# Kernel optimization log

Hardware: AMD Instinct MI355X
Metric: run time of the kernel (lower is better)

Reference implementation:

```python
import jax, jax.numpy as jnp
import numpy as np

N_USERS = 100000
N_ITEMS = 50000
N_NODES = N_USERS + N_ITEMS
EMB_DIM = 64
N_EDGES = 4000000
N_LAYERS = 3
BATCH = 4096


def setup_inputs() -> dict:
    key = jax.random.key(0)
    k = jax.random.split(key, 7)
    return {
        "user_emb": jax.random.normal(k[0], (N_USERS, EMB_DIM), dtype=jnp.float32) * 0.1,
        "item_emb": jax.random.normal(k[1], (N_ITEMS, EMB_DIM), dtype=jnp.float32) * 0.1,
        "vals": jax.random.uniform(k[2], (N_EDGES,), dtype=jnp.float32),
        "src": jax.random.randint(k[3], (N_EDGES,), 0, N_NODES, dtype=jnp.int32),
        "dst": jax.random.randint(k[4], (N_EDGES,), 0, N_NODES, dtype=jnp.int32),
        "users": jax.random.randint(k[5], (BATCH,), 0, N_USERS, dtype=jnp.int32),
        "items": jax.random.randint(k[6], (BATCH,), 0, N_ITEMS, dtype=jnp.int32),
    }


def _propagate(user_emb, item_emb, vals, src, dst):
    # all_emb: [N, D]; sparse adjacency A given as COO (src -> dst, weight vals)
    all_emb = jnp.concatenate([user_emb, item_emb], axis=0)
    acc = all_emb  # running sum over layers (layer 0 included)
    emb = all_emb
    for _ in range(N_LAYERS):
        # SpMM: out[d] = sum_{e: dst[e]==d} vals[e] * emb[src[e]]
        msgs = vals[:, None] * emb[src]               # [E, D]
        emb = jax.ops.segment_sum(msgs, dst, num_segments=N_NODES)
        acc = acc + emb
    light_out = acc / jnp.float32(N_LAYERS + 1)       # mean over stacked layers
    return light_out[:N_USERS], light_out[N_USERS:]


def reference(user_emb, item_emb, vals, src, dst, users, items):
    all_users, all_items = _propagate(user_emb, item_emb, vals, src, dst)
    u = all_users[users]                              # [B, D]
    i = all_items[items]                              # [B, D]
    gamma = jnp.sum(u * i, axis=1)                    # [B]
    return gamma
```

## Files before the change

kernel.cpp:

```cpp
#include <hip/hip_runtime.h>
#include <hip/hip_bf16.h>

#define N_USERS 100000
#define N_ITEMS 50000
#define N_NODES 150000
#define DIM 64
#define N_EDGES 4000000
#define BATCH 4096

#define NBKT 512
#define BW 294
#define STRIDE 9216
#define PA_EDGES 4096
#define PA_ITER 16
#define PA_BLOCKS ((N_EDGES + PA_EDGES - 1) / PA_EDGES)
#define CVT_BLOCKS (N_NODES * DIM / 4 / 256)

__device__ __forceinline__ float blo(unsigned int u) { return __uint_as_float(u << 16); }
__device__ __forceinline__ float bhi(unsigned int u) { return __uint_as_float(u & 0xffff0000u); }
__device__ __forceinline__ unsigned int f2b(float f) {
    unsigned int x = __float_as_uint(f);
    return (x + 0x7fffu + ((x >> 16) & 1u)) >> 16;
}
__device__ __forceinline__ unsigned int pack2(float a, float b) {
    return f2b(a) | (f2b(b) << 16);
}

typedef float v2f __attribute__((ext_vector_type(2)));

__global__ void __launch_bounds__(256, 4) k_cvtpart(
        const float* __restrict__ uemb, const float* __restrict__ iemb,
        ushort* __restrict__ ebf0,
        const int* __restrict__ src, const int* __restrict__ dst,
        const float* __restrict__ vals,
        int* __restrict__ gcur, int2* __restrict__ tmp) {
    __shared__ int cnt[NBKT];
    __shared__ int base_s[NBKT];
    __shared__ int off_s[NBKT];
    __shared__ int2 rec_s[PA_EDGES];
    __shared__ ushort bin_s[PA_EDGES];
    int t = threadIdx.x;
    if (blockIdx.x >= PA_BLOCKS) {
        int tid = (blockIdx.x - PA_BLOCKS) * 256 + t;
        int i = tid * 4;
        if (i >= N_NODES * DIM) return;
        const float* srcp = (i < N_USERS * DIM) ? (uemb + i) : (iemb + (i - N_USERS * DIM));
        float4 v;
        v.x = __builtin_nontemporal_load(srcp + 0);
        v.y = __builtin_nontemporal_load(srcp + 1);
        v.z = __builtin_nontemporal_load(srcp + 2);
        v.w = __builtin_nontemporal_load(srcp + 3);
        *(uint2*)(ebf0 + i) = make_uint2(pack2(v.x, v.y), pack2(v.z, v.w));
        return;
    }
    for (int i = t; i < NBKT; i += 256) cnt[i] = 0;
    __syncthreads();
    size_t base = (size_t)blockIdx.x * PA_EDGES;
    int myb[PA_ITER];
    int mykey[PA_ITER];
    int myval[PA_ITER];
#pragma unroll
    for (int it = 0; it < PA_ITER; it++) {
        size_t i = base + (size_t)it * 256 + t;
        myb[it] = -1;
        if (i < N_EDGES) {
            int d = __builtin_nontemporal_load(dst + i);
            int s = __builtin_nontemporal_load(src + i);
            float v = __builtin_nontemporal_load(vals + i);
            int b = d / BW;
            int local = d - b * BW;
            myb[it] = b;
            mykey[it] = (s << 9) | local;
            myval[it] = __float_as_int(v);
            atomicAdd(&cnt[b], 1);
        }
    }
    __syncthreads();
    for (int i = t; i < NBKT; i += 256) {
        int c = cnt[i];
        base_s[i] = (c > 0) ? atomicAdd(&gcur[i], c) : 0;
    }
    if (t < 64) {
        int lane = t;
        int carry = 0;
        for (int c = 0; c < NBKT / 64; c++) {
            int i = c * 64 + lane;
            int x = cnt[i];
            int incl = x;
            for (int o = 1; o < 64; o <<= 1) {
                int y = __shfl_up(incl, o);
                if (lane >= o) incl += y;
            }
            off_s[i] = carry + incl - x;
            carry += __shfl(incl, 63);
        }
    }
    __syncthreads();
    for (int i = t; i < NBKT; i += 256) cnt[i] = 0;
    __syncthreads();
#pragma unroll
    for (int it = 0; it < PA_ITER; it++) {
        int b = myb[it];
        if (b >= 0) {
            int pos = off_s[b] + atomicAdd(&cnt[b], 1);
            rec_s[pos] = make_int2(mykey[it], myval[it]);
            bin_s[pos] = (ushort)b;
        }
    }
    __syncthreads();
    int nrec = off_s[NBKT - 1] + cnt[NBKT - 1];
    for (int i = t; i < nrec; i += 256) {
        int2 r = rec_s[i];
        int b = bin_s[i];
        tmp[(size_t)b * STRIDE + base_s[b] + (i - off_s[b])] = r;
    }
}

__global__ void k_bsort(const int2* __restrict__ tmp, const int* __restrict__ gcur,
                        int* __restrict__ row_ptr, int2* __restrict__ fin) {
    __shared__ int cnt[BW + 64];
    __shared__ int off[BW + 64];
    __shared__ int gbase_s;
    int b = blockIdx.x, t = threadIdx.x;
    int node0 = b * BW;
    int nodes = min(BW, N_NODES - node0);
    int count = gcur[b];
    const int2* tb = tmp + (size_t)b * STRIDE;
    if (t < 64) {
        int ssum = 0;
#pragma unroll
        for (int j = 0; j < 8; j++) {
            int idx = t * 8 + j;
            if (idx < b) ssum += gcur[idx];
        }
        for (int o = 32; o; o >>= 1) ssum += __shfl_xor(ssum, o);
        if (t == 0) gbase_s = ssum;
    }
    for (int i = t; i < BW + 64; i += 512) cnt[i] = 0;
    __syncthreads();
    int gbase = gbase_s;
    for (int e = t; e < count; e += 512) atomicAdd(&cnt[tb[e].x & 511], 1);
    __syncthreads();
    if (t < 64) {
        int lane = t;
        int carry = 0;
        for (int c = 0; c < 5; c++) {
            int i = c * 64 + lane;
            int x = (i < nodes) ? cnt[i] : 0;
            int incl = x;
            for (int o = 1; o < 64; o <<= 1) {
                int y = __shfl_up(incl, o);
                if (lane >= o) incl += y;
            }
            if (i <= nodes) off[i] = carry + incl - x;
            carry += __shfl(incl, 63);
        }
    }
    __syncthreads();
    for (int i = t; i <= nodes; i += 512)
        if (node0 + i <= N_NODES) row_ptr[node0 + i] = gbase + off[i];
    __syncthreads();
    for (int e = t; e < count; e += 512) {
        int2 r = tb[e];
        int local = r.x & 511;
        int pos = gbase + atomicAdd(&off[local], 1);
        fin[pos] = make_int2(r.x >> 9, r.y);
    }
}


#define EDGE_FMA(r, u, A0, A1, A2, A3)                                        \
    {                                                                         \
        float vf = __int_as_float((r).y);                                     \
        v2f vv = {vf, vf};                                                    \
        v2f f0 = {blo((u).x), bhi((u).x)};                                    \
        v2f f1 = {blo((u).y), bhi((u).y)};                                    \
        v2f f2 = {blo((u).z), bhi((u).z)};                                    \
        v2f f3 = {blo((u).w), bhi((u).w)};                                    \
        A0 = __builtin_elementwise_fma(vv, f0, A0);                           \
        A1 = __builtin_elementwise_fma(vv, f1, A1);                           \
        A2 = __builtin_elementwise_fma(vv, f2, A2);                           \
        A3 = __builtin_elementwise_fma(vv, f3, A3);                           \
    }

#define GATHER16(basec, r) (*(const uint4*)((basec) + ((((unsigned int)(r).x) << 7) | qoff)))
#define REC8(basec, i) (*(const int2*)((basec) + (((unsigned int)(i)) << 3)))

__global__ void __launch_bounds__(256) k_spmm16(
        const ushort* __restrict__ ein, ushort* __restrict__ eout,
        const int* __restrict__ row_ptr, const int2* __restrict__ fin) {
    int wave = (blockIdx.x * blockDim.x + threadIdx.x) >> 6;
    if (wave >= N_NODES / 2) return;
    int lane = threadIdx.x & 63;
    int g = lane >> 3;
    int q = lane & 7;
    unsigned int qoff = (unsigned int)q << 4;
    const char* einc = (const char*)ein;
    const char* finc = (const char*)fin;
    int n0 = wave * 2;
    int s0 = row_ptr[n0];
    int m0 = row_ptr[n0 + 1];
    int m1 = row_ptr[n0 + 2];
    int last0 = max(s0, m0 - 1);
    int last1 = max(m0, m1 - 1);
    v2f A0 = {0.f, 0.f}, A1 = {0.f, 0.f}, A2 = {0.f, 0.f}, A3 = {0.f, 0.f};
    v2f B0 = {0.f, 0.f}, B1 = {0.f, 0.f}, B2 = {0.f, 0.f}, B3 = {0.f, 0.f};
    int ea = s0 + g, eb = m0 + g;
    while (ea < m0 || eb < m1) {
        int2 ra0 = REC8(finc, min(ea, last0));
        int2 ra1 = REC8(finc, min(ea + 8, last0));
        int2 ra2 = REC8(finc, min(ea + 16, last0));
        int2 ra3 = REC8(finc, min(ea + 24, last0));
        int2 rb0 = REC8(finc, min(eb, last1));
        int2 rb1 = REC8(finc, min(eb + 8, last1));
        int2 rb2 = REC8(finc, min(eb + 16, last1));
        int2 rb3 = REC8(finc, min(eb + 24, last1));
        ra0.y = (ea < m0) ? ra0.y : 0;
        ra1.y = (ea + 8 < m0) ? ra1.y : 0;
        ra2.y = (ea + 16 < m0) ? ra2.y : 0;
        ra3.y = (ea + 24 < m0) ? ra3.y : 0;
        rb0.y = (eb < m1) ? rb0.y : 0;
        rb1.y = (eb + 8 < m1) ? rb1.y : 0;
        rb2.y = (eb + 16 < m1) ? rb2.y : 0;
        rb3.y = (eb + 24 < m1) ? rb3.y : 0;
        uint4 ua0 = GATHER16(einc, ra0);
        uint4 ua1 = GATHER16(einc, ra1);
        uint4 ua2 = GATHER16(einc, ra2);
        uint4 ua3 = GATHER16(einc, ra3);
        uint4 ub0 = GATHER16(einc, rb0);
        uint4 ub1 = GATHER16(einc, rb1);
        uint4 ub2 = GATHER16(einc, rb2);
        uint4 ub3 = GATHER16(einc, rb3);
        EDGE_FMA(ra0, ua0, A0, A1, A2, A3);
        EDGE_FMA(ra1, ua1, A0, A1, A2, A3);
        EDGE_FMA(ra2, ua2, A0, A1, A2, A3);
        EDGE_FMA(ra3, ua3, A0, A1, A2, A3);
        EDGE_FMA(rb0, ub0, B0, B1, B2, B3);
        EDGE_FMA(rb1, ub1, B0, B1, B2, B3);
        EDGE_FMA(rb2, ub2, B0, B1, B2, B3);
        EDGE_FMA(rb3, ub3, B0, B1, B2, B3);
        ea += 32;
        eb += 32;
    }
#pragma unroll
    for (int off = 8; off < 64; off <<= 1) {
        A0.x += __shfl_xor(A0.x, off);
        A0.y += __shfl_xor(A0.y, off);
        A1.x += __shfl_xor(A1.x, off);
        A1.y += __shfl_xor(A1.y, off);
        A2.x += __shfl_xor(A2.x, off);
        A2.y += __shfl_xor(A2.y, off);
        A3.x += __shfl_xor(A3.x, off);
        A3.y += __shfl_xor(A3.y, off);
        B0.x += __shfl_xor(B0.x, off);
        B0.y += __shfl_xor(B0.y, off);
        B1.x += __shfl_xor(B1.x, off);
        B1.y += __shfl_xor(B1.y, off);
        B2.x += __shfl_xor(B2.x, off);
        B2.y += __shfl_xor(B2.y, off);
        B3.x += __shfl_xor(B3.x, off);
        B3.y += __shfl_xor(B3.y, off);
    }
    if (lane < 16) {
        bool r0 = lane < 8;
        uint4 p;
        p.x = r0 ? pack2(A0.x, A0.y) : pack2(B0.x, B0.y);
        p.y = r0 ? pack2(A1.x, A1.y) : pack2(B1.x, B1.y);
        p.z = r0 ? pack2(A2.x, A2.y) : pack2(B2.x, B2.y);
        p.w = r0 ? pack2(A3.x, A3.y) : pack2(B3.x, B3.y);
        *(uint4*)(eout + (size_t)n0 * DIM + (size_t)(lane & 15) * 8) = p;
    }
}

__global__ void k_samp(const ushort* __restrict__ ein, const int* __restrict__ row_ptr,
                       const int2* __restrict__ fin, const int* __restrict__ users,
                       const int* __restrict__ items, float* __restrict__ l3) {
    int slot = (blockIdx.x * blockDim.x + threadIdx.x) >> 6;
    if (slot >= 2 * BATCH) return;
    int lane = threadIdx.x & 63;
    int g = lane >> 3;
    int q = lane & 7;
    unsigned int qoff = (unsigned int)q << 4;
    const char* einc = (const char*)ein;
    const char* finc = (const char*)fin;
    int node = (slot < BATCH) ? users[slot] : (items[slot - BATCH] + N_USERS);
    int start = row_ptr[node], end = row_ptr[node + 1];
    int last = max(start, end - 1);
    v2f A0 = {0.f, 0.f}, A1 = {0.f, 0.f}, A2 = {0.f, 0.f}, A3 = {0.f, 0.f};
    int e = start + g;
    while (e < end) {
        int e1 = e + 8, e2 = e + 16, e3 = e + 24;
        int2 ra = REC8(finc, e);
        int2 rb = REC8(finc, min(e1, last));
        int2 rc = REC8(finc, min(e2, last));
        int2 rd = REC8(finc, min(e3, last));
        rb.y = (e1 < end) ? rb.y : 0;
        rc.y = (e2 < end) ? rc.y : 0;
        rd.y = (e3 < end) ? rd.y : 0;
        uint4 ua = GATHER16(einc, ra);
        uint4 ub = GATHER16(einc, rb);
        uint4 uc = GATHER16(einc, rc);
        uint4 ud = GATHER16(einc, rd);
        EDGE_FMA(ra, ua, A0, A1, A2, A3);
        EDGE_FMA(rb, ub, A0, A1, A2, A3);
        EDGE_FMA(rc, uc, A0, A1, A2, A3);
        EDGE_FMA(rd, ud, A0, A1, A2, A3);
        e += 32;
    }
#pragma unroll
    for (int off = 8; off < 64; off <<= 1) {
        A0.x += __shfl_xor(A0.x, off);
        A0.y += __shfl_xor(A0.y, off);
        A1.x += __shfl_xor(A1.x, off);
        A1.y += __shfl_xor(A1.y, off);
        A2.x += __shfl_xor(A2.x, off);
        A2.y += __shfl_xor(A2.y, off);
        A3.x += __shfl_xor(A3.x, off);
        A3.y += __shfl_xor(A3.y, off);
    }
    if (lane < 8) {
        float* row = l3 + (size_t)slot * DIM + q * 8;
        *(float4*)row = make_float4(A0.x, A0.y, A1.x, A1.y);
        *(float4*)(row + 4) = make_float4(A2.x, A2.y, A3.x, A3.y);
    }
}

__global__ void k_gacc0(const float* __restrict__ uemb, const float* __restrict__ iemb,
                        const ushort* __restrict__ emb, const int* __restrict__ users,
                        const int* __restrict__ items, float* __restrict__ accU,
                        float* __restrict__ accI) {
    int i = blockIdx.x * blockDim.x + threadIdx.x;
    if (i >= 2 * BATCH * DIM) return;
    int j = (i < BATCH * DIM) ? i : i - BATCH * DIM;
    int b = j >> 6, l = j & 63;
    if (i < BATCH * DIM) {
        int n = users[b];
        unsigned int u = emb[(size_t)n * DIM + l];
        accU[j] = uemb[(size_t)n * DIM + l] + __uint_as_float(u << 16);
    } else {
        int n = items[b];
        unsigned int u = emb[(size_t)(n + N_USERS) * DIM + l];
        accI[j] = iemb[(size_t)n * DIM + l] + __uint_as_float(u << 16);
    }
}

__global__ void k_gacc(const ushort* __restrict__ emb, const int* __restrict__ users,
                       const int* __restrict__ items, float* __restrict__ accU,
                       float* __restrict__ accI) {
    int i = blockIdx.x * blockDim.x + threadIdx.x;
    if (i >= 2 * BATCH * DIM) return;
    int j = (i < BATCH * DIM) ? i : i - BATCH * DIM;
    int b = j >> 6, l = j & 63;
    if (i < BATCH * DIM) {
        unsigned int u = emb[(size_t)users[b] * DIM + l];
        accU[j] += __uint_as_float(u << 16);
    } else {
        unsigned int u = emb[(size_t)(items[b] + N_USERS) * DIM + l];
        accI[j] += __uint_as_float(u << 16);
    }
}

__global__ void k_dot(const float* __restrict__ accU, const float* __restrict__ accI,
                      const float* __restrict__ l3, float* __restrict__ out) {
    int b = (blockIdx.x * blockDim.x + threadIdx.x) >> 6;
    if (b >= BATCH) return;
    int lane = threadIdx.x & 63;
    float aU = accU[b * 64 + lane] + l3[(size_t)b * 64 + lane];
    float aI = accI[b * 64 + lane] + l3[(size_t)(BATCH + b) * 64 + lane];
    float p = aU * aI;
    for (int off = 32; off; off >>= 1) p += __shfl_xor(p, off);
    if (lane == 0) out[b] = p * (1.0f / 16.0f);
}


extern "C" void kernel_launch(void* const* d_in, const int* in_sizes, int n_in,
                              void* d_out, int out_size, void* d_ws, size_t ws_size,
                              hipStream_t stream) {
    const float* user_emb = (const float*)d_in[0];
    const float* item_emb = (const float*)d_in[1];
    const float* vals = (const float*)d_in[2];
    const int* src = (const int*)d_in[3];
    const int* dst = (const int*)d_in[4];
    const int* users = (const int*)d_in[5];
    const int* items = (const int*)d_in[6];
    float* out = (float*)d_out;

    char* ws = (char*)d_ws;
    size_t off = 0;
    auto alloc = [&](size_t bytes) {
        char* p = ws + off;
        off += (bytes + 255) & ~(size_t)255;
        return p;
    };
    ushort* ebf0 = (ushort*)alloc((size_t)N_NODES * DIM * 2);
    ushort* ebf1 = (ushort*)alloc((size_t)N_NODES * DIM * 2);
    ushort* ebf2 = (ushort*)alloc((size_t)N_NODES * DIM * 2);
    int2* fin = (int2*)alloc((size_t)N_EDGES * 8);
    int* row_ptr = (int*)alloc((size_t)(N_NODES + 1) * 4);
    int* gcur = (int*)alloc((size_t)NBKT * 4);
    float* l3 = (float*)alloc((size_t)2 * BATCH * DIM * 4);
    float* accU = (float*)alloc((size_t)BATCH * DIM * 4);
    float* accI = (float*)alloc((size_t)BATCH * DIM * 4);
    int2* tmp = (int2*)ebf1;

    hipMemsetAsync(gcur, 0, (size_t)NBKT * 4, stream);

    k_cvtpart<<<PA_BLOCKS + CVT_BLOCKS, 256, 0, stream>>>(
        user_emb, item_emb, ebf0, src, dst, vals, gcur, tmp);
    k_bsort<<<NBKT, 512, 0, stream>>>(tmp, gcur, row_ptr, fin);

    int gb = (2 * BATCH * DIM + 255) / 256;
    int spmm_blocks = (N_NODES / 2 * 64 + 255) / 256;
    k_spmm16<<<spmm_blocks, 256, 0, stream>>>(ebf0, ebf1, row_ptr, fin);
    k_gacc0<<<gb, 256, 0, stream>>>(user_emb, item_emb, ebf1, users, items, accU, accI);
    k_spmm16<<<spmm_blocks, 256, 0, stream>>>(ebf1, ebf2, row_ptr, fin);
    k_gacc<<<gb, 256, 0, stream>>>(ebf2, users, items, accU, accI);
    k_samp<<<(2 * BATCH * 64 + 255) / 256, 256, 0, stream>>>(ebf2, row_ptr, fin, users, items, l3);

    k_dot<<<(BATCH * 64 + 255) / 256, 256, 0, stream>>>(accU, accI, l3, out);
}
```

Measured before the change: 338.9 us.

## Preload edge records before sync in partition/sort and use one node per wave in SpMM

The partition kernel now issues all global loads of dst/src/vals before clearing the shared counters and syncing, so memory latency overlaps the setup. The bucket sort kernel caches up to 16 records per thread in registers, so the tmp buffer is read once instead of twice. The SpMM kernel goes from two nodes per wave to one node per wave, with twice as many blocks, which cuts register pressure and avoids imbalance between paired rows. In exchange, each wave has fewer independent gathers in flight and more waves must be scheduled.

```diff
diff --git a/kernel.cpp b/kernel.cpp
--- a/kernel.cpp
+++ b/kernel.cpp
@@ -15,6 +15,7 @@
 #define PA_ITER 16
 #define PA_BLOCKS ((N_EDGES + PA_EDGES - 1) / PA_EDGES)
 #define CVT_BLOCKS (N_NODES * DIM / 4 / 256)
+#define BS_ITER 16
 
 __device__ __forceinline__ float blo(unsigned int u) { return __uint_as_float(u << 16); }
 __device__ __forceinline__ float bhi(unsigned int u) { return __uint_as_float(u & 0xffff0000u); }
@@ -53,25 +54,30 @@
         *(uint2*)(ebf0 + i) = make_uint2(pack2(v.x, v.y), pack2(v.z, v.w));
         return;
     }
-    for (int i = t; i < NBKT; i += 256) cnt[i] = 0;
-    __syncthreads();
-    size_t base = (size_t)blockIdx.x * PA_EDGES;
     int myb[PA_ITER];
     int mykey[PA_ITER];
     int myval[PA_ITER];
+    size_t base = (size_t)blockIdx.x * PA_EDGES;
 #pragma unroll
     for (int it = 0; it < PA_ITER; it++) {
         size_t i = base + (size_t)it * 256 + t;
-        myb[it] = -1;
         if (i < N_EDGES) {
-            int d = __builtin_nontemporal_load(dst + i);
-            int s = __builtin_nontemporal_load(src + i);
-            float v = __builtin_nontemporal_load(vals + i);
+            myb[it] = __builtin_nontemporal_load(dst + i);
+            mykey[it] = __builtin_nontemporal_load(src + i);
+            myval[it] = __float_as_int(__builtin_nontemporal_load(vals + i));
+        } else {
+            myb[it] = -1;
+        }
+    }
+    for (int i = t; i < NBKT; i += 256) cnt[i] = 0;
+    __syncthreads();
+#pragma unroll
+    for (int it = 0; it < PA_ITER; it++) {
+        int d = myb[it];
+        if (d >= 0) {
             int b = d / BW;
-            int local = d - b * BW;
+            mykey[it] = (mykey[it] << 9) | (d - b * BW);
             myb[it] = b;
-            mykey[it] = (s << 9) | local;
-            myval[it] = __float_as_int(v);
             atomicAdd(&cnt[b], 1);
         }
     }
@@ -126,6 +132,12 @@
     int nodes = min(BW, N_NODES - node0);
     int count = gcur[b];
     const int2* tb = tmp + (size_t)b * STRIDE;
+    int2 myrec[BS_ITER];
+#pragma unroll
+    for (int it = 0; it < BS_ITER; it++) {
+        int e = it * 512 + t;
+        myrec[it] = (e < count) ? tb[e] : make_int2(-1, 0);
+    }
     if (t < 64) {
         int ssum = 0;
 #pragma unroll
@@ -139,7 +151,11 @@
     for (int i = t; i < BW + 64; i += 512) cnt[i] = 0;
     __syncthreads();
     int gbase = gbase_s;
-    for (int e = t; e < count; e += 512) atomicAdd(&cnt[tb[e].x & 511], 1);
+#pragma unroll
+    for (int it = 0; it < BS_ITER; it++)
+        if (myrec[it].x >= 0) atomicAdd(&cnt[myrec[it].x & 511], 1);
+    for (int e = BS_ITER * 512 + t; e < count; e += 512)
+        atomicAdd(&cnt[tb[e].x & 511], 1);
     __syncthreads();
     if (t < 64) {
         int lane = t;
@@ -160,10 +176,17 @@
     for (int i = t; i <= nodes; i += 512)
         if (node0 + i <= N_NODES) row_ptr[node0 + i] = gbase + off[i];
     __syncthreads();
-    for (int e = t; e < count; e += 512) {
+#pragma unroll
+    for (int it = 0; it < BS_ITER; it++) {
+        int2 r = myrec[it];
+        if (r.x >= 0) {
+            int pos = gbase + atomicAdd(&off[r.x & 511], 1);
+            fin[pos] = make_int2(r.x >> 9, r.y);
+        }
+    }
+    for (int e = BS_ITER * 512 + t; e < count; e += 512) {
         int2 r = tb[e];
-        int local = r.x & 511;
-        int pos = gbase + atomicAdd(&off[local], 1);
+        int pos = gbase + atomicAdd(&off[r.x & 511], 1);
         fin[pos] = make_int2(r.x >> 9, r.y);
     }
 }
@@ -186,62 +209,42 @@
 #define GATHER16(basec, r) (*(const uint4*)((basec) + ((((unsigned int)(r).x) << 7) | qoff)))
 #define REC8(basec, i) (*(const int2*)((basec) + (((unsigned int)(i)) << 3)))
 
-__global__ void __launch_bounds__(256) k_spmm16(
-        const ushort* __restrict__ ein, ushort* __restrict__ eout,
-        const int* __restrict__ row_ptr, const int2* __restrict__ fin) {
+#define BURST32(basec)                                                        \
+    {                                                                         \
+        int e1 = e + 8, e2 = e + 16, e3 = e + 24;                             \
+        int2 ra = REC8(basec, e);                                             \
+        int2 rb = REC8(basec, min(e1, last));                                 \
+        int2 rc = REC8(basec, min(e2, last));                                 \
+        int2 rd = REC8(basec, min(e3, last));                                 \
+        rb.y = (e1 < end) ? rb.y : 0;                                         \
+        rc.y = (e2 < end) ? rc.y : 0;                                         \
+        rd.y = (e3 < end) ? rd.y : 0;                                         \
+        uint4 ua = GATHER16(einc, ra);                                        \
+        uint4 ub = GATHER16(einc, rb);                                        \
+        uint4 uc = GATHER16(einc, rc);                                        \
+        uint4 ud = GATHER16(einc, rd);                                        \
+        EDGE_FMA(ra, ua, A0, A1, A2, A3);                                     \
+        EDGE_FMA(rb, ub, A0, A1, A2, A3);                                     \
+        EDGE_FMA(rc, uc, A0, A1, A2, A3);                                     \
+        EDGE_FMA(rd, ud, A0, A1, A2, A3);                                     \
+        e += 32;                                                              \
+    }
+
+__global__ void k_spmm16(const ushort* __restrict__ ein, ushort* __restrict__ eout,
+                         const int* __restrict__ row_ptr, const int2* __restrict__ fin) {
     int wave = (blockIdx.x * blockDim.x + threadIdx.x) >> 6;
-    if (wave >= N_NODES / 2) return;
+    if (wave >= N_NODES) return;
     int lane = threadIdx.x & 63;
     int g = lane >> 3;
     int q = lane & 7;
     unsigned int qoff = (unsigned int)q << 4;
     const char* einc = (const char*)ein;
     const char* finc = (const char*)fin;
-    int n0 = wave * 2;
-    int s0 = row_ptr[n0];
-    int m0 = row_ptr[n0 + 1];
-    int m1 = row_ptr[n0 + 2];
-    int last0 = max(s0, m0 - 1);
-    int last1 = max(m0, m1 - 1);
+    int start = row_ptr[wave], end = row_ptr[wave + 1];
+    int last = max(start, end - 1);
     v2f A0 = {0.f, 0.f}, A1 = {0.f, 0.f}, A2 = {0.f, 0.f}, A3 = {0.f, 0.f};
-    v2f B0 = {0.f, 0.f}, B1 = {0.f, 0.f}, B2 = {0.f, 0.f}, B3 = {0.f, 0.f};
-    int ea = s0 + g, eb = m0 + g;
-    while (ea < m0 || eb < m1) {
-        int2 ra0 = REC8(finc, min(ea, last0));
-        int2 ra1 = REC8(finc, min(ea + 8, last0));
-        int2 ra2 = REC8(finc, min(ea + 16, last0));
-        int2 ra3 = REC8(finc, min(ea + 24, last0));
-        int2 rb0 = REC8(finc, min(eb, last1));
-        int2 rb1 = REC8(finc, min(eb + 8, last1));
-        int2 rb2 = REC8(finc, min(eb + 16, last1));
-        int2 rb3 = REC8(finc, min(eb + 24, last1));
-        ra0.y = (ea < m0) ? ra0.y : 0;
-        ra1.y = (ea + 8 < m0) ? ra1.y : 0;
-        ra2.y = (ea + 16 < m0) ? ra2.y : 0;
-        ra3.y = (ea + 24 < m0) ? ra3.y : 0;
-        rb0.y = (eb < m1) ? rb0.y : 0;
-        rb1.y = (eb + 8 < m1) ? rb1.y : 0;
-        rb2.y = (eb + 16 < m1) ? rb2.y : 0;
-        rb3.y = (eb + 24 < m1) ? rb3.y : 0;
-        uint4 ua0 = GATHER16(einc, ra0);
-        uint4 ua1 = GATHER16(einc, ra1);
-        uint4 ua2 = GATHER16(einc, ra2);
-        uint4 ua3 = GATHER16(einc, ra3);
-        uint4 ub0 = GATHER16(einc, rb0);
-        uint4 ub1 = GATHER16(einc, rb1);
-        uint4 ub2 = GATHER16(einc, rb2);
-        uint4 ub3 = GATHER16(einc, rb3);
-        EDGE_FMA(ra0, ua0, A0, A1, A2, A3);
-        EDGE_FMA(ra1, ua1, A0, A1, A2, A3);
-        EDGE_FMA(ra2, ua2, A0, A1, A2, A3);
-        EDGE_FMA(ra3, ua3, A0, A1, A2, A3);
-        EDGE_FMA(rb0, ub0, B0, B1, B2, B3);
-        EDGE_FMA(rb1, ub1, B0, B1, B2, B3);
-        EDGE_FMA(rb2, ub2, B0, B1, B2, B3);
-        EDGE_FMA(rb3, ub3, B0, B1, B2, B3);
-        ea += 32;
-        eb += 32;
-    }
+    int e = start + g;
+    while (e < end) BURST32(finc);
 #pragma unroll
     for (int off = 8; off < 64; off <<= 1) {
         A0.x += __shfl_xor(A0.x, off);
@@ -252,23 +255,14 @@
         A2.y += __shfl_xor(A2.y, off);
         A3.x += __shfl_xor(A3.x, off);
         A3.y += __shfl_xor(A3.y, off);
-        B0.x += __shfl_xor(B0.x, off);
-        B0.y += __shfl_xor(B0.y, off);
-        B1.x += __shfl_xor(B1.x, off);
-        B1.y += __shfl_xor(B1.y, off);
-        B2.x += __shfl_xor(B2.x, off);
-        B2.y += __shfl_xor(B2.y, off);
-        B3.x += __shfl_xor(B3.x, off);
-        B3.y += __shfl_xor(B3.y, off);
-    }
-    if (lane < 16) {
-        bool r0 = lane < 8;
+    }
+    if (lane < 8) {
         uint4 p;
-        p.x = r0 ? pack2(A0.x, A0.y) : pack2(B0.x, B0.y);
-        p.y = r0 ? pack2(A1.x, A1.y) : pack2(B1.x, B1.y);
-        p.z = r0 ? pack2(A2.x, A2.y) : pack2(B2.x, B2.y);
-        p.w = r0 ? pack2(A3.x, A3.y) : pack2(B3.x, B3.y);
-        *(uint4*)(eout + (size_t)n0 * DIM + (size_t)(lane & 15) * 8) = p;
+        p.x = pack2(A0.x, A0.y);
+        p.y = pack2(A1.x, A1.y);
+        p.z = pack2(A2.x, A2.y);
+        p.w = pack2(A3.x, A3.y);
+        *(uint4*)(eout + (size_t)wave * DIM + q * 8) = p;
     }
 }
 
@@ -288,25 +282,7 @@
     int last = max(start, end - 1);
     v2f A0 = {0.f, 0.f}, A1 = {0.f, 0.f}, A2 = {0.f, 0.f}, A3 = {0.f, 0.f};
     int e = start + g;
-    while (e < end) {
-        int e1 = e + 8, e2 = e + 16, e3 = e + 24;
-        int2 ra = REC8(finc, e);
-        int2 rb = REC8(finc, min(e1, last));
-        int2 rc = REC8(finc, min(e2, last));
-        int2 rd = REC8(finc, min(e3, last));
-        rb.y = (e1 < end) ? rb.y : 0;
-        rc.y = (e2 < end) ? rc.y : 0;
-        rd.y = (e3 < end) ? rd.y : 0;
-        uint4 ua = GATHER16(einc, ra);
-        uint4 ub = GATHER16(einc, rb);
-        uint4 uc = GATHER16(einc, rc);
-        uint4 ud = GATHER16(einc, rd);
-        EDGE_FMA(ra, ua, A0, A1, A2, A3);
-        EDGE_FMA(rb, ub, A0, A1, A2, A3);
-        EDGE_FMA(rc, uc, A0, A1, A2, A3);
-        EDGE_FMA(rd, ud, A0, A1, A2, A3);
-        e += 32;
-    }
+    while (e < end) BURST32(finc);
 #pragma unroll
     for (int off = 8; off < 64; off <<= 1) {
         A0.x += __shfl_xor(A0.x, off);
@@ -410,7 +386,7 @@
     k_bsort<<<NBKT, 512, 0, stream>>>(tmp, gcur, row_ptr, fin);
 
     int gb = (2 * BATCH * DIM + 255) / 256;
-    int spmm_blocks = (N_NODES / 2 * 64 + 255) / 256;
+    int spmm_blocks = (N_NODES * 64 + 255) / 256;
     k_spmm16<<<spmm_blocks, 256, 0, stream>>>(ebf0, ebf1, row_ptr, fin);
     k_gacc0<<<gb, 256, 0, stream>>>(user_emb, item_emb, ebf1, users, items, accU, accI);
     k_spmm16<<<spmm_blocks, 256, 0, stream>>>(ebf1, ebf2, row_ptr, fin);
```

Result: faster. 327.2 us (-3.5%).
